# Performance work log

Measured on AMD Instinct MI355X. Metric: run time of the kernel, lower is better.

## Reference

```python
import jax, jax.numpy as jnp
import numpy as np

D_MODEL = 1024
N_INPUT = 4096
N_PROCESS = 2048
D_ROUTING = 256
TEMPERATURE = 0.5
LN_EPS = 1e-5


def _gelu(x):
    return jax.nn.gelu(x, approximate=False)  # torch F.gelu default (erf)


def setup_inputs() -> dict:
    key = jax.random.key(0)
    ks = jax.random.split(key, 10)
    B, S = 8, 2048
    x = jax.random.normal(ks[0], (B, S, D_MODEL), dtype=jnp.float32)
    # GlobalRouter query_net: Linear(d_model, 2*d_routing) -> GELU -> LayerNorm -> Linear(2*d_routing, d_routing)
    W1 = jax.random.normal(ks[1], (2 * D_ROUTING, D_MODEL), dtype=jnp.float32) * (2.0 / (D_MODEL + 2 * D_ROUTING)) ** 0.5 * 1.414
    b1 = jnp.zeros((2 * D_ROUTING,), dtype=jnp.float32)
    ln_g = jnp.ones((2 * D_ROUTING,), dtype=jnp.float32)
    ln_b = jnp.zeros((2 * D_ROUTING,), dtype=jnp.float32)
    W2 = jax.random.normal(ks[2], (D_ROUTING, 2 * D_ROUTING), dtype=jnp.float32) * (2.0 / (3 * D_ROUTING)) ** 0.5 * 1.414
    b2 = jnp.zeros((D_ROUTING,), dtype=jnp.float32)
    neuron_keys = jax.random.normal(ks[3], (N_INPUT, D_ROUTING), dtype=jnp.float32) / D_ROUTING ** 0.5 * 1.414
    input_patterns = jax.random.normal(ks[4], (N_INPUT, D_MODEL), dtype=jnp.float32) / D_MODEL ** 0.5 * 1.414
    process_weights = jax.random.normal(ks[5], (N_PROCESS, N_INPUT), dtype=jnp.float32) / N_INPUT ** 0.5 * 1.414
    process_outputs = jax.random.normal(ks[6], (N_PROCESS, D_MODEL), dtype=jnp.float32) / D_MODEL ** 0.5 * 1.414
    return {
        'x': x, 'k_input': 2048, 'k_process': 1024,
        'W1': W1, 'b1': b1, 'ln_g': ln_g, 'ln_b': ln_b, 'W2': W2, 'b2': b2,
        'neuron_keys': neuron_keys, 'input_patterns': input_patterns,
        'process_weights': process_weights, 'process_outputs': process_outputs,
    }


def _forward(x, k_input, k_process, W1, b1, ln_g, ln_b, W2, b2,
             neuron_keys, input_patterns, process_weights, process_outputs):
    B, S, d_model = x.shape
    # ---- GlobalRouter ----
    gctx = jnp.max(x, axis=1)                                  # [B, d_model]
    h = _gelu(gctx @ W1.T + b1)                                # [B, 2*d_routing]
    mu = jnp.mean(h, axis=-1, keepdims=True)
    var = jnp.mean((h - mu) ** 2, axis=-1, keepdims=True)
    h = (h - mu) * jax.lax.rsqrt(var + LN_EPS) * ln_g + ln_b
    query = h @ W2.T + b2                                      # [B, d_routing]
    logits = (query @ neuron_keys.T) / D_ROUTING ** 0.5        # [B, n_input]
    probs = jax.nn.softmax(logits / TEMPERATURE, axis=-1)
    _, input_idx = jax.lax.top_k(logits, k_input)              # [B, k_input]
    one_hot = jnp.zeros_like(probs).at[jnp.arange(B)[:, None], input_idx].set(1.0)
    routing_weights = jax.lax.stop_gradient(one_hot - probs) + probs  # STE
    # ---- input neuron stage ----
    input_acts = _gelu(jnp.einsum('bsd,nd->bsn', x, input_patterns))   # [B,S,n_input]
    weighted = input_acts * routing_weights[:, None, :]
    sel_in = jnp.take_along_axis(weighted, input_idx[:, None, :], axis=2)  # [B,S,k_input]
    # gather process weight columns per batch: [B, n_process, k_input]
    W_sel = jnp.transpose(process_weights[:, input_idx], (1, 0, 2))
    process_acts = _gelu(jnp.einsum('bsk,bpk->bsp', sel_in, W_sel))    # [B,S,n_process]
    # ---- process neuron stage ----
    process_scores = jnp.mean(process_acts, axis=1)                    # [B,n_process]
    _, process_idx = jax.lax.top_k(process_scores, k_process)          # [B,k_process]
    sel_proc = jnp.take_along_axis(process_acts, process_idx[:, None, :], axis=2)  # [B,S,k_process]
    out_sel = process_outputs[process_idx]                             # [B,k_process,d_model]
    return jnp.einsum('bsp,bpd->bsd', sel_proc, out_sel)


def reference(x, k_input, k_process, W1, b1, ln_g, ln_b, W2, b2,
              neuron_keys, input_patterns, process_weights, process_outputs):
    return _forward(x, k_input, k_process, W1, b1, ln_g, ln_b, W2, b2,
                    neuron_keys, input_patterns, process_weights, process_outputs)
```

## Files before the change

### kernel.cpp

```cpp
#include <hip/hip_runtime.h>
#include <stdint.h>

#define B_  8
#define S_  2048
#define DM  1024
#define NI  4096
#define NP  2048
#define DR  256
#define H2  512
#define KI  2048
#define KP  1024
#define LDW 40

typedef __attribute__((ext_vector_type(8))) short bf16x8;
typedef __attribute__((ext_vector_type(4))) float f32x4;
typedef unsigned short ushort;
typedef unsigned int uint;

__device__ __forceinline__ float gelu_erf(float v){
    return 0.5f * v * (1.0f + erff(v * 0.7071067811865476f));
}
__device__ __forceinline__ ushort f2b(float f){
    union { float f; uint u; } a; a.f = f;
    uint r = a.u + 0x7fffu + ((a.u >> 16) & 1u);
    return (ushort)(r >> 16);
}
__device__ __forceinline__ float b2f(ushort u){
    union { uint u; float f; } a; a.u = ((uint)u) << 16; return a.f;
}
__device__ __forceinline__ void cvt8(const float* p, uint4& H, uint4& L){
    uint h[4], l[4];
    #pragma unroll
    for(int i = 0; i < 4; i++){
        ushort h0 = f2b(p[2*i]);   float f0 = b2f(h0); ushort l0 = f2b(p[2*i]   - f0);
        ushort h1 = f2b(p[2*i+1]); float f1 = b2f(h1); ushort l1 = f2b(p[2*i+1] - f1);
        h[i] = (uint)h0 | ((uint)h1 << 16);
        l[i] = (uint)l0 | ((uint)l1 << 16);
    }
    H = uint4{h[0],h[1],h[2],h[3]};
    L = uint4{l[0],l[1],l[2],l[3]};
}
__device__ __forceinline__ void gload_lds16(const void* g, void* l){
    __builtin_amdgcn_global_load_lds((const __attribute__((address_space(1))) void*)g,
                                     (__attribute__((address_space(3))) void*)l, 16, 0, 0);
}

__global__ __launch_bounds__(256) void k_pre(const float* __restrict__ x,
                                             const float* __restrict__ patt,
                                             const float* __restrict__ pout,
                                             float* __restrict__ gpart,
                                             ushort* __restrict__ xh,
                                             ushort* __restrict__ xl,
                                             ushort* __restrict__ patth,
                                             ushort* __restrict__ pattl,
                                             ushort* __restrict__ poutb){
    int bid = blockIdx.x;
    int t = threadIdx.x;
    if(bid < 256){
        int b = bid >> 5, ch = bid & 31;
        size_t row0 = (size_t)b*S_ + (size_t)ch*64;
        const float4* xb = (const float4*)(x + row0*DM);
        float4 m = float4{-3.402823466e38f, -3.402823466e38f, -3.402823466e38f, -3.402823466e38f};
        for(int r = 0; r < 64; r++){
            float4 v = xb[(size_t)r*(DM/4) + t];
            ushort hx = f2b(v.x), hy = f2b(v.y), hz = f2b(v.z), hw = f2b(v.w);
            uint2 H{ (uint)hx | ((uint)hy << 16), (uint)hz | ((uint)hw << 16) };
            uint2 L{ (uint)f2b(v.x - b2f(hx)) | ((uint)f2b(v.y - b2f(hy)) << 16),
                     (uint)f2b(v.z - b2f(hz)) | ((uint)f2b(v.w - b2f(hw)) << 16) };
            ((uint2*)(xh + (row0 + r)*DM))[t] = H;
            ((uint2*)(xl + (row0 + r)*DM))[t] = L;
            m.x = fmaxf(m.x, v.x); m.y = fmaxf(m.y, v.y);
            m.z = fmaxf(m.z, v.z); m.w = fmaxf(m.w, v.w);
        }
        ((float4*)(gpart + (size_t)(b*32 + ch)*DM))[t] = m;
    }else if(bid < 2304){
        size_t idx = (size_t)(bid - 256)*256 + t;
        float f[8];
        *(float4*)(f)     = ((const float4*)patt)[idx*2];
        *(float4*)(f + 4) = ((const float4*)patt)[idx*2 + 1];
        uint4 H, L; cvt8(f, H, L);
        ((uint4*)patth)[idx] = H;
        ((uint4*)pattl)[idx] = L;
    }else{
        size_t idx = (size_t)(bid - 2304)*256 + t;
        float f[8];
        *(float4*)(f)     = ((const float4*)pout)[idx*2];
        *(float4*)(f + 4) = ((const float4*)pout)[idx*2 + 1];
        uint o[4];
        #pragma unroll
        for(int i = 0; i < 4; i++)
            o[i] = (uint)f2b(f[2*i]) | ((uint)f2b(f[2*i+1]) << 16);
        ((uint4*)poutb)[idx] = uint4{o[0], o[1], o[2], o[3]};
    }
}

__global__ __launch_bounds__(256) void k_h(const float* __restrict__ gpart,
                                           const float* __restrict__ W1,
                                           const float* __restrict__ b1,
                                           float* __restrict__ h){
    __shared__ float g[DM];
    int b = blockIdx.x >> 3, ig = blockIdx.x & 7;
    int t = threadIdx.x;
    for(int d = t; d < DM; d += 256){
        float m = gpart[(size_t)(b*32)*DM + d];
        for(int c = 1; c < 32; c++) m = fmaxf(m, gpart[(size_t)(b*32 + c)*DM + d]);
        g[d] = m;
    }
    __syncthreads();
    int i  = ig*64 + (t >> 2);
    int dq = (t & 3) * 256;
    const float* wr = W1 + (size_t)i*DM + dq;
    const float* gg = g + dq;
    float s = 0.f;
    for(int d = 0; d < 256; d++) s = fmaf(gg[d], wr[d], s);
    s += __shfl_xor(s, 1);
    s += __shfl_xor(s, 2);
    if((t & 3) == 0) h[b*H2 + i] = gelu_erf(s + b1[i]);
}

__global__ __launch_bounds__(256) void k_query(const float* __restrict__ h,
                                               const float* __restrict__ lng,
                                               const float* __restrict__ lnb,
                                               const float* __restrict__ W2,
                                               const float* __restrict__ b2,
                                               float* __restrict__ query){
    __shared__ float hn[H2];
    __shared__ float red[4];
    int b = blockIdx.x >> 2, qg = blockIdx.x & 3;
    int t = threadIdx.x;
    float v0 = h[b*H2 + t], v1 = h[b*H2 + 256 + t];
    float s = v0 + v1;
    for(int o = 32; o > 0; o >>= 1) s += __shfl_down(s, o);
    if((t & 63) == 0) red[t >> 6] = s;
    __syncthreads();
    float mean = (red[0] + red[1] + red[2] + red[3]) * (1.f/H2);
    __syncthreads();
    float d0 = v0 - mean, d1 = v1 - mean;
    float sq = d0*d0 + d1*d1;
    for(int o = 32; o > 0; o >>= 1) sq += __shfl_down(sq, o);
    if((t & 63) == 0) red[t >> 6] = sq;
    __syncthreads();
    float var  = (red[0] + red[1] + red[2] + red[3]) * (1.f/H2);
    float rstd = rsqrtf(var + 1e-5f);
    hn[t]       = d0*rstd*lng[t]       + lnb[t];
    hn[256 + t] = d1*rstd*lng[256 + t] + lnb[256 + t];
    __syncthreads();
    int q  = qg*64 + (t >> 2);
    int iq = (t & 3) * 128;
    const float* wr = W2 + (size_t)q*H2 + iq;
    float acc = 0.f;
    for(int i2 = 0; i2 < 128; i2++) acc = fmaf(hn[iq + i2], wr[i2], acc);
    acc += __shfl_xor(acc, 1);
    acc += __shfl_xor(acc, 2);
    if((t & 3) == 0) query[b*DR + q] = acc + b2[q];
}

__global__ __launch_bounds__(256) void k_logits(const float* __restrict__ query,
                                                const float* __restrict__ nk,
                                                float* __restrict__ logits){
    __shared__ float4 q4[DR/4];
    int b = blockIdx.x >> 5, ng = blockIdx.x & 31;
    int t = threadIdx.x;
    if(t < 64) q4[t] = ((const float4*)(query + (size_t)b*DR))[t];
    __syncthreads();
    int w = t >> 6, lane = t & 63;
    float4 qv = q4[lane];
    int nbase = ng*128 + w*32;
    #pragma unroll 2
    for(int i = 0; i < 32; i++){
        int n = nbase + i;
        float4 v = ((const float4*)(nk + (size_t)n*DR))[lane];
        float p = v.x*qv.x + v.y*qv.y + v.z*qv.z + v.w*qv.w;
        p += __shfl_down(p, 32); p += __shfl_down(p, 16); p += __shfl_down(p, 8);
        p += __shfl_down(p, 4);  p += __shfl_down(p, 2);  p += __shfl_down(p, 1);
        if(lane == 0) logits[(size_t)b*NI + n] = p * 0.0625f;
    }
}

template<int N_, int KSEL>
__global__ __launch_bounds__(1024) void k_topk(const float* __restrict__ vals,
                                               int* __restrict__ idxout){
    __shared__ unsigned u[N_];
    __shared__ int hist[256];
    __shared__ int sfx[512];
    __shared__ int sc[1024];
    __shared__ int sel_d, sel_need;
    int t = threadIdx.x;
    size_t vbase = (size_t)blockIdx.x * N_;
    size_t obase = (size_t)blockIdx.x * KSEL;
    for(int i = t; i < N_; i += 1024){
        unsigned bits = __float_as_uint(vals[vbase + i]);
        u[i] = (bits & 0x80000000u) ? ~bits : (bits | 0x80000000u);
    }
    unsigned long long prefix = 0;
    int need = KSEL;
    for(int bb = 3; bb >= 0; bb--){
        if(t < 256) hist[t] = 0;
        __syncthreads();
        for(int i = t; i < N_; i += 1024){
            unsigned v = u[i];
            if(((unsigned long long)v >> ((bb + 1)*8)) == prefix)
                atomicAdd(&hist[(v >> (bb*8)) & 255], 1);
        }
        __syncthreads();
        if(t < 256) sfx[t] = hist[t];
        else if(t < 512) sfx[t] = 0;
        __syncthreads();
        for(int o = 1; o < 256; o <<= 1){
            int v2 = (t < 256) ? sfx[t + o] : 0;
            __syncthreads();
            if(t < 256) sfx[t] += v2;
            __syncthreads();
        }
        if(t < 256){
            int hi_c = sfx[t + 1];
            if(sfx[t] >= need && hi_c < need){ sel_d = t; sel_need = need - hi_c; }
        }
        __syncthreads();
        prefix = (prefix << 8) | (unsigned)sel_d;
        need = sel_need;
        __syncthreads();
    }
    unsigned T = (unsigned)prefix;
    const int PER = N_ / 1024;
    int base = t * PER;
    int lgt = 0, leq = 0;
    for(int j = 0; j < PER; j++){
        unsigned v = u[base + j];
        lgt += (v > T) ? 1 : 0; leq += (v == T) ? 1 : 0;
    }
    sc[t] = (lgt << 16) | leq;
    __syncthreads();
    for(int o = 1; o < 1024; o <<= 1){
        int add = (t >= o) ? sc[t - o] : 0;
        __syncthreads();
        sc[t] += add;
        __syncthreads();
    }
    int need2 = KSEL - (sc[1023] >> 16);
    int ex = (t == 0) ? 0 : sc[t - 1];
    int pos = (ex >> 16) + ((ex & 0xffff) < need2 ? (ex & 0xffff) : need2);
    int eq = ex & 0xffff;
    for(int j = 0; j < PER; j++){
        unsigned v = u[base + j];
        if(v > T){ idxout[obase + pos++] = base + j; }
        else if(v == T){ if(eq < need2){ idxout[obase + pos++] = base + j; } eq++; }
    }
}

__global__ __launch_bounds__(256) void k_gemm1(const ushort* __restrict__ xh,
                                               const ushort* __restrict__ xl,
                                               const ushort* __restrict__ ph,
                                               const ushort* __restrict__ pl,
                                               const int* __restrict__ iidx,
                                               ushort* __restrict__ selh,
                                               ushort* __restrict__ sell, int b0){
    __shared__ __align__(16) ushort Ah[2][128*32], Al[2][128*32], Bh[2][128*32], Bl[2][128*32];
    __shared__ int rowmap[128];
    int t = threadIdx.x;
    int g = blockIdx.x >> 8, rest = blockIdx.x & 255;
    int b = b0 + g;
    int mb = rest >> 4, nb = rest & 15;
    int m0 = mb*128, n0 = nb*128;
    ushort* selh_g = selh + (size_t)g*S_*KI;
    ushort* sell_g = sell + (size_t)g*S_*KI;
    if(t < 128) rowmap[t] = iidx[(size_t)b*KI + n0 + t];
    __syncthreads();
    int w = t >> 6, l = t & 63;
    int lr = l >> 2, lc = l & 3;
    int r0 = 32*w + lr, r1 = r0 + 16;
    const ushort* pAh0 = xh + ((size_t)b*S_ + m0 + r0)*DM + lc*8;
    const ushort* pAh1 = xh + ((size_t)b*S_ + m0 + r1)*DM + lc*8;
    const ushort* pAl0 = xl + ((size_t)b*S_ + m0 + r0)*DM + lc*8;
    const ushort* pAl1 = xl + ((size_t)b*S_ + m0 + r1)*DM + lc*8;
    const ushort* pBh0 = ph + (size_t)rowmap[r0]*DM + lc*8;
    const ushort* pBh1 = ph + (size_t)rowmap[r1]*DM + lc*8;
    const ushort* pBl0 = pl + (size_t)rowmap[r0]*DM + lc*8;
    const ushort* pBl1 = pl + (size_t)rowmap[r1]*DM + lc*8;
    int d0 = w*1024, d1 = d0 + 512;
    #define STG1(BUF, KO) do{ \
        gload_lds16(pAh0 + (KO), &Ah[BUF][d0]); \
        gload_lds16(pAh1 + (KO), &Ah[BUF][d1]); \
        gload_lds16(pAl0 + (KO), &Al[BUF][d0]); \
        gload_lds16(pAl1 + (KO), &Al[BUF][d1]); \
        gload_lds16(pBh0 + (KO), &Bh[BUF][d0]); \
        gload_lds16(pBh1 + (KO), &Bh[BUF][d1]); \
        gload_lds16(pBl0 + (KO), &Bl[BUF][d0]); \
        gload_lds16(pBl1 + (KO), &Bl[BUF][d1]); \
    }while(0)
    STG1(0, 0);
    int lm = l & 15, q = l >> 4;
    int mbase = (w >> 1)*64, nbase = (w & 1)*64;
    f32x4 acc[4][4];
    #pragma unroll
    for(int i = 0; i < 4; i++)
      #pragma unroll
      for(int j = 0; j < 4; j++) acc[i][j] = f32x4{0.f,0.f,0.f,0.f};
    int cur = 0;
    for(int k0 = 0; k0 < DM; k0 += 32){
        if(k0 + 32 < DM){
            STG1(cur^1, k0 + 32);
            asm volatile("s_waitcnt vmcnt(8)" ::: "memory");
        }else{
            asm volatile("s_waitcnt vmcnt(0)" ::: "memory");
        }
        __builtin_amdgcn_s_barrier();
        asm volatile("" ::: "memory");
        bf16x8 ahf[4], alf[4];
        #pragma unroll
        for(int mt = 0; mt < 4; mt++){
            ahf[mt] = *(const bf16x8*)(&Ah[cur][(mbase + mt*16 + lm)*32 + q*8]);
            alf[mt] = *(const bf16x8*)(&Al[cur][(mbase + mt*16 + lm)*32 + q*8]);
        }
        __builtin_amdgcn_s_setprio(1);
        #pragma unroll
        for(int nt = 0; nt < 4; nt++){
            bf16x8 bhf = *(const bf16x8*)(&Bh[cur][(nbase + nt*16 + lm)*32 + q*8]);
            bf16x8 blf = *(const bf16x8*)(&Bl[cur][(nbase + nt*16 + lm)*32 + q*8]);
            #pragma unroll
            for(int mt = 0; mt < 4; mt++){
                acc[mt][nt] = __builtin_amdgcn_mfma_f32_16x16x32_bf16(ahf[mt], bhf, acc[mt][nt], 0, 0, 0);
                acc[mt][nt] = __builtin_amdgcn_mfma_f32_16x16x32_bf16(ahf[mt], blf, acc[mt][nt], 0, 0, 0);
                acc[mt][nt] = __builtin_amdgcn_mfma_f32_16x16x32_bf16(alf[mt], bhf, acc[mt][nt], 0, 0, 0);
            }
        }
        __builtin_amdgcn_s_setprio(0);
        asm volatile("s_waitcnt lgkmcnt(0)" ::: "memory");
        __builtin_amdgcn_s_barrier();
        asm volatile("" ::: "memory");
        cur ^= 1;
    }
    #undef STG1
    #pragma unroll
    for(int mt = 0; mt < 4; mt++)
      #pragma unroll
      for(int nt = 0; nt < 4; nt++){
        int col = n0 + nbase + nt*16 + lm;
        #pragma unroll
        for(int i = 0; i < 4; i++){
            int row = m0 + mbase + mt*16 + q*4 + i;
            float gv = gelu_erf(acc[mt][nt][i]);
            ushort hbits = f2b(gv);
            selh_g[(size_t)row*KI + col] = hbits;
            sell_g[(size_t)row*KI + col] = f2b(gv - b2f(hbits));
        }
      }
}

__global__ __launch_bounds__(256) void k_gather_wsel(const float* __restrict__ pw,
                                                     const int* __restrict__ iidx,
                                                     ushort* __restrict__ wh,
                                                     ushort* __restrict__ wl,
                                                     float* __restrict__ scores, int b0){
    int g = blockIdx.x >> 8, pc = blockIdx.x & 255;
    int b = b0 + g;
    ushort* wh_g = wh + (size_t)g*NP*KI;
    ushort* wl_g = wl + (size_t)g*NP*KI;
    int t = threadIdx.x;
    if(t < 8) scores[(size_t)b*NP + pc*8 + t] = 0.f;
    int j0 = t*8;
    int k8[8];
    *(int4*)(k8)     = *(const int4*)(iidx + (size_t)b*KI + j0);
    *(int4*)(k8 + 4) = *(const int4*)(iidx + (size_t)b*KI + j0 + 4);
    for(int r2 = 0; r2 < 8; r2++){
        int p = pc*8 + r2;
        const float* row = pw + (size_t)p*NI;
        uint hh[4], ll[4];
        #pragma unroll
        for(int i = 0; i < 4; i++){
            float v0 = row[k8[2*i]], v1 = row[k8[2*i+1]];
            ushort h0 = f2b(v0), h1 = f2b(v1);
            hh[i] = (uint)h0 | ((uint)h1 << 16);
            ll[i] = (uint)f2b(v0 - b2f(h0)) | ((uint)f2b(v1 - b2f(h1)) << 16);
        }
        *(uint4*)(wh_g + (size_t)p*KI + j0) = uint4{hh[0],hh[1],hh[2],hh[3]};
        *(uint4*)(wl_g + (size_t)p*KI + j0) = uint4{ll[0],ll[1],ll[2],ll[3]};
    }
}

__global__ __launch_bounds__(256) void k_gemm2(const ushort* __restrict__ selh,
                                               const ushort* __restrict__ sell,
                                               const ushort* __restrict__ wh,
                                               const ushort* __restrict__ wl,
                                               ushort* __restrict__ acts,
                                               float* __restrict__ scores, int b0){
    __shared__ __align__(16) ushort Ah[2][128*32], Al[2][128*32], Bh[2][128*32], Bl[2][128*32];
    __shared__ float colsum[128];
    int t = threadIdx.x;
    int g = blockIdx.x >> 8, rest = blockIdx.x & 255;
    int b = b0 + g;
    int mb = rest >> 4, nb = rest & 15;
    int m0 = mb*128, n0 = nb*128;
    const ushort* selh_g = selh + (size_t)g*S_*KI;
    const ushort* sell_g = sell + (size_t)g*S_*KI;
    const ushort* wh_g   = wh   + (size_t)g*NP*KI;
    const ushort* wl_g   = wl   + (size_t)g*NP*KI;
    ushort* acts_g = acts + (size_t)g*S_*NP;
    int w = t >> 6, l = t & 63;
    int lr = l >> 2, lc = l & 3;
    int r0 = 32*w + lr, r1 = r0 + 16;
    const ushort* pAh0 = selh_g + (size_t)(m0 + r0)*KI + lc*8;
    const ushort* pAh1 = selh_g + (size_t)(m0 + r1)*KI + lc*8;
    const ushort* pAl0 = sell_g + (size_t)(m0 + r0)*KI + lc*8;
    const ushort* pAl1 = sell_g + (size_t)(m0 + r1)*KI + lc*8;
    const ushort* pBh0 = wh_g + (size_t)(n0 + r0)*KI + lc*8;
    const ushort* pBh1 = wh_g + (size_t)(n0 + r1)*KI + lc*8;
    const ushort* pBl0 = wl_g + (size_t)(n0 + r0)*KI + lc*8;
    const ushort* pBl1 = wl_g + (size_t)(n0 + r1)*KI + lc*8;
    int d0 = w*1024, d1 = d0 + 512;
    #define STG2(BUF, KO) do{ \
        gload_lds16(pAh0 + (KO), &Ah[BUF][d0]); \
        gload_lds16(pAh1 + (KO), &Ah[BUF][d1]); \
        gload_lds16(pAl0 + (KO), &Al[BUF][d0]); \
        gload_lds16(pAl1 + (KO), &Al[BUF][d1]); \
        gload_lds16(pBh0 + (KO), &Bh[BUF][d0]); \
        gload_lds16(pBh1 + (KO), &Bh[BUF][d1]); \
        gload_lds16(pBl0 + (KO), &Bl[BUF][d0]); \
        gload_lds16(pBl1 + (KO), &Bl[BUF][d1]); \
    }while(0)
    STG2(0, 0);
    int lm = l & 15, q = l >> 4;
    int mbase = (w >> 1)*64, nbase = (w & 1)*64;
    f32x4 acc[4][4];
    #pragma unroll
    for(int i = 0; i < 4; i++)
      #pragma unroll
      for(int j = 0; j < 4; j++) acc[i][j] = f32x4{0.f,0.f,0.f,0.f};
    int cur = 0;
    for(int k0 = 0; k0 < KI; k0 += 32){
        if(k0 + 32 < KI){
            STG2(cur^1, k0 + 32);
            asm volatile("s_waitcnt vmcnt(8)" ::: "memory");
        }else{
            asm volatile("s_waitcnt vmcnt(0)" ::: "memory");
        }
        __builtin_amdgcn_s_barrier();
        asm volatile("" ::: "memory");
        bf16x8 ahf[4], alf[4];
        #pragma unroll
        for(int mt = 0; mt < 4; mt++){
            ahf[mt] = *(const bf16x8*)(&Ah[cur][(mbase + mt*16 + lm)*32 + q*8]);
            alf[mt] = *(const bf16x8*)(&Al[cur][(mbase + mt*16 + lm)*32 + q*8]);
        }
        __builtin_amdgcn_s_setprio(1);
        #pragma unroll
        for(int nt = 0; nt < 4; nt++){
            bf16x8 bhf = *(const bf16x8*)(&Bh[cur][(nbase + nt*16 + lm)*32 + q*8]);
            bf16x8 blf = *(const bf16x8*)(&Bl[cur][(nbase + nt*16 + lm)*32 + q*8]);
            #pragma unroll
            for(int mt = 0; mt < 4; mt++){
                acc[mt][nt] = __builtin_amdgcn_mfma_f32_16x16x32_bf16(ahf[mt], bhf, acc[mt][nt], 0, 0, 0);
                acc[mt][nt] = __builtin_amdgcn_mfma_f32_16x16x32_bf16(ahf[mt], blf, acc[mt][nt], 0, 0, 0);
                acc[mt][nt] = __builtin_amdgcn_mfma_f32_16x16x32_bf16(alf[mt], bhf, acc[mt][nt], 0, 0, 0);
            }
        }
        __builtin_amdgcn_s_setprio(0);
        asm volatile("s_waitcnt lgkmcnt(0)" ::: "memory");
        __builtin_amdgcn_s_barrier();
        asm volatile("" ::: "memory");
        cur ^= 1;
    }
    #undef STG2
    if(t < 128) colsum[t] = 0.f;
    __syncthreads();
    #pragma unroll
    for(int mt = 0; mt < 4; mt++)
      #pragma unroll
      for(int nt = 0; nt < 4; nt++){
        int cb = nbase + nt*16 + lm;
        float s4 = 0.f;
        #pragma unroll
        for(int i = 0; i < 4; i++){
            int row = m0 + mbase + mt*16 + q*4 + i;
            float gv = gelu_erf(acc[mt][nt][i]);
            s4 += gv;
            acts_g[(size_t)row*NP + n0 + cb] = f2b(gv);
        }
        atomicAdd(&colsum[cb], s4);
      }
    __syncthreads();
    if(t < 128) atomicAdd(&scores[(size_t)b*NP + n0 + t], colsum[t]);
}

__global__ __launch_bounds__(256) void k_gather_selacts(const ushort* __restrict__ acts,
                                                        const int* __restrict__ pidx,
                                                        ushort* __restrict__ selacts, int b0){
    int g = blockIdx.x >> 6, sc_ = blockIdx.x & 63;
    int b = b0 + g;
    const ushort* acts_g = acts + (size_t)g*S_*NP;
    ushort* selacts_g = selacts + (size_t)g*S_*KP;
    int t = threadIdx.x;
    int j0 = t*4;
    int4 p4 = *(const int4*)(pidx + (size_t)b*KP + j0);
    const ushort* Ab = acts_g    + ((size_t)sc_*32)*NP;
    ushort*       Ob = selacts_g + ((size_t)sc_*32)*KP;
    for(int r2 = 0; r2 < 32; r2++){
        const ushort* Ar = Ab + (size_t)r2*NP;
        ushort o0 = Ar[p4.x], o1 = Ar[p4.y], o2 = Ar[p4.z], o3 = Ar[p4.w];
        uint2 ov{ (uint)o0 | ((uint)o1 << 16), (uint)o2 | ((uint)o3 << 16) };
        *(uint2*)(Ob + (size_t)r2*KP + j0) = ov;
    }
}

__global__ __launch_bounds__(256) void k_gemm3(const ushort* __restrict__ selacts,
                                               const ushort* __restrict__ poutb,
                                               const int* __restrict__ pidx,
                                               float* __restrict__ out, int b0){
    __shared__ __align__(16) ushort As[2][128*32];
    __shared__ __align__(16) ushort Bs[2][128*LDW];
    __shared__ int pix[KP];
    int t = threadIdx.x;
    int g = blockIdx.x >> 7, rest = blockIdx.x & 127;
    int b = b0 + g;
    int mb = rest >> 3, nb = rest & 7;
    int m0 = mb*128, n0 = nb*128;
    const ushort* sel_g = selacts + (size_t)g*S_*KP;
    int w = t >> 6, l = t & 63;
    int lr = l >> 2, lc = l & 3;
    int r0 = 32*w + lr, r1 = r0 + 16;
    const ushort* pA0 = sel_g + (size_t)(m0 + r0)*KP + lc*8;
    const ushort* pA1 = sel_g + (size_t)(m0 + r1)*KP + lc*8;
    int d0 = w*1024, d1 = d0 + 512;
    gload_lds16(pA0, &As[0][d0]);
    gload_lds16(pA1, &As[0][d1]);
    for(int i = t; i < KP; i += 256) pix[i] = pidx[(size_t)b*KP + i];
    __syncthreads();
    int kk = t >> 3, nc = (t & 7)*16;
    uint4 B0, B1;
    {
        const ushort* bg = poutb + (size_t)pix[kk]*DM + n0 + nc;
        B0 = *(const uint4*)(bg); B1 = *(const uint4*)(bg + 8);
    }
    int lm = l & 15, q = l >> 4;
    int mbase = (w >> 1)*64, nbase = (w & 1)*64;
    f32x4 acc[4][4];
    #pragma unroll
    for(int i = 0; i < 4; i++)
      #pragma unroll
      for(int j = 0; j < 4; j++) acc[i][j] = f32x4{0.f,0.f,0.f,0.f};
    for(int k0 = 0; k0 < KP; k0 += 32){
        int cur = (k0 >> 5) & 1;
        {
            const ushort* pb0 = (const ushort*)&B0;
            const ushort* pb1 = (const ushort*)&B1;
            #pragma unroll
            for(int c = 0; c < 8; c++) Bs[cur][(nc + c)*LDW + kk]     = pb0[c];
            #pragma unroll
            for(int c = 0; c < 8; c++) Bs[cur][(nc + 8 + c)*LDW + kk] = pb1[c];
        }
        if(k0 + 32 < KP){
            gload_lds16(pA0 + (k0 + 32), &As[cur^1][d0]);
            gload_lds16(pA1 + (k0 + 32), &As[cur^1][d1]);
            asm volatile("s_waitcnt vmcnt(2)" ::: "memory");
        }else{
            asm volatile("s_waitcnt vmcnt(0)" ::: "memory");
        }
        asm volatile("s_waitcnt lgkmcnt(0)" ::: "memory");
        __builtin_amdgcn_s_barrier();
        asm volatile("" ::: "memory");
        if(k0 + 32 < KP){
            const ushort* bg = poutb + (size_t)pix[k0 + 32 + kk]*DM + n0 + nc;
            B0 = *(const uint4*)(bg); B1 = *(const uint4*)(bg + 8);
        }
        bf16x8 af[4];
        #pragma unroll
        for(int mt = 0; mt < 4; mt++)
            af[mt] = *(const bf16x8*)(&As[cur][(mbase + mt*16 + lm)*32 + q*8]);
        __builtin_amdgcn_s_setprio(1);
        #pragma unroll
        for(int nt = 0; nt < 4; nt++){
            bf16x8 bf = *(const bf16x8*)(&Bs[cur][(nbase + nt*16 + lm)*LDW + q*8]);
            #pragma unroll
            for(int mt = 0; mt < 4; mt++)
                acc[mt][nt] = __builtin_amdgcn_mfma_f32_16x16x32_bf16(af[mt], bf, acc[mt][nt], 0, 0, 0);
        }
        __builtin_amdgcn_s_setprio(0);
        asm volatile("s_waitcnt lgkmcnt(0)" ::: "memory");
        __builtin_amdgcn_s_barrier();
        asm volatile("" ::: "memory");
    }
    float* Cb = out + (size_t)b*S_*DM;
    #pragma unroll
    for(int mt = 0; mt < 4; mt++)
      #pragma unroll
      for(int nt = 0; nt < 4; nt++){
        int col = n0 + nbase + nt*16 + lm;
        #pragma unroll
        for(int i = 0; i < 4; i++){
            int row = m0 + mbase + mt*16 + q*4 + i;
            Cb[(size_t)row*DM + col] = acc[mt][nt][i];
        }
      }
}

extern "C" void kernel_launch(void* const* d_in, const int* in_sizes, int n_in,
                              void* d_out, int out_size, void* d_ws, size_t ws_size,
                              hipStream_t stream){
    const float* x    = (const float*)d_in[0];
    const float* W1   = (const float*)d_in[3];
    const float* b1   = (const float*)d_in[4];
    const float* lng  = (const float*)d_in[5];
    const float* lnb  = (const float*)d_in[6];
    const float* W2   = (const float*)d_in[7];
    const float* b2   = (const float*)d_in[8];
    const float* nk   = (const float*)d_in[9];
    const float* patt = (const float*)d_in[10];
    const float* pw   = (const float*)d_in[11];
    const float* pout = (const float*)d_in[12];
    float* out = (float*)d_out;

    auto al256 = [](size_t v){ return (v + 255) & ~(size_t)255; };
    const size_t fixed =
        al256((size_t)B_*32*DM*4) + al256((size_t)B_*H2*4) + al256((size_t)B_*DR*4) +
        al256((size_t)B_*NI*4)    + al256((size_t)B_*KI*4) + al256((size_t)B_*NP*4) +
        al256((size_t)B_*KP*4) +
        2*al256((size_t)B_*S_*DM*2) + 2*al256((size_t)NI*DM*2) + al256((size_t)NP*DM*2);
    const size_t perb = (size_t)S_*KI*2*2 + (size_t)NP*KI*2*2 + (size_t)S_*NP*2 + (size_t)S_*KP*2 + 6*256;
    int G = 8;
    while(G > 1 && fixed + (size_t)G*perb > ws_size) G >>= 1;
    if(fixed + (size_t)G*perb > ws_size) return;

    char* wsp = (char*)d_ws;
    size_t off = 0;
    auto alloc = [&](size_t bytes) -> void* {
        void* p = wsp + off;
        off += (bytes + 255) & ~(size_t)255;
        return p;
    };
    float*  gpart   = (float*) alloc((size_t)B_*32*DM*4);
    float*  h       = (float*) alloc((size_t)B_*H2*4);
    float*  query   = (float*) alloc((size_t)B_*DR*4);
    float*  logits  = (float*) alloc((size_t)B_*NI*4);
    int*    iidx    = (int*)   alloc((size_t)B_*KI*4);
    float*  scores  = (float*) alloc((size_t)B_*NP*4);
    int*    pidx    = (int*)   alloc((size_t)B_*KP*4);
    ushort* xh      = (ushort*)alloc((size_t)B_*S_*DM*2);
    ushort* xl      = (ushort*)alloc((size_t)B_*S_*DM*2);
    ushort* patth   = (ushort*)alloc((size_t)NI*DM*2);
    ushort* pattl   = (ushort*)alloc((size_t)NI*DM*2);
    ushort* poutb   = (ushort*)alloc((size_t)NP*DM*2);
    ushort* selh    = (ushort*)alloc((size_t)G*S_*KI*2);
    ushort* sell    = (ushort*)alloc((size_t)G*S_*KI*2);
    ushort* wselh   = (ushort*)alloc((size_t)G*NP*KI*2);
    ushort* wsell   = (ushort*)alloc((size_t)G*NP*KI*2);
    ushort* acts    = (ushort*)alloc((size_t)G*S_*NP*2);
    ushort* selacts = (ushort*)alloc((size_t)G*S_*KP*2);

    dim3 blk(256);
    k_pre   <<<3328, blk, 0, stream>>>(x, patt, pout, gpart, xh, xl, patth, pattl, poutb);
    k_h     <<<64,  blk, 0, stream>>>(gpart, W1, b1, h);
    k_query <<<32,  blk, 0, stream>>>(h, lng, lnb, W2, b2, query);
    k_logits<<<B_*32, blk, 0, stream>>>(query, nk, logits);
    k_topk<NI, KI><<<B_, dim3(1024), 0, stream>>>(logits, iidx);
    for(int b0 = 0; b0 < B_; b0 += G){
        k_gemm1        <<<G*256, blk, 0, stream>>>(xh, xl, patth, pattl, iidx, selh, sell, b0);
        k_gather_wsel  <<<G*256, blk, 0, stream>>>(pw, iidx, wselh, wsell, scores, b0);
        k_gemm2        <<<G*256, blk, 0, stream>>>(selh, sell, wselh, wsell, acts, scores, b0);
        k_topk<NP, KP> <<<G,     dim3(1024), 0, stream>>>(scores + (size_t)b0*NP, pidx + (size_t)b0*KP);
        k_gather_selacts<<<G*64, blk, 0, stream>>>(acts, pidx, selacts, b0);
        k_gemm3        <<<G*128, blk, 0, stream>>>(selacts, poutb, pidx, out, b0);
    }
}
```

Baseline: 1.334 ms.

## Widen gemm1/gemm2 tiles to 128x256 with XOR-swizzled LDS layout

The first two split-bf16 GEMMs now use 128x256 block tiles, with each wave owning a 128x64 strip instead of a 64x64 quadrant. This halves the grid and raises operand reuse per LDS load. LDS rows are XOR-swizzled on both the global-to-LDS staging and the fragment reads, to reduce bank conflicts. In exchange, the block uses roughly double the LDS and 128 accumulator registers per lane with launch_bounds(256,1), which lowers occupancy, and there are fewer blocks to spread across CUs.

```diff
diff --git a/kernel.cpp b/kernel.cpp
--- a/kernel.cpp
+++ b/kernel.cpp
@@ -248,80 +248,90 @@
     }
 }
 
-__global__ __launch_bounds__(256) void k_gemm1(const ushort* __restrict__ xh,
-                                               const ushort* __restrict__ xl,
-                                               const ushort* __restrict__ ph,
-                                               const ushort* __restrict__ pl,
-                                               const int* __restrict__ iidx,
-                                               ushort* __restrict__ selh,
-                                               ushort* __restrict__ sell, int b0){
-    __shared__ __align__(16) ushort Ah[2][128*32], Al[2][128*32], Bh[2][128*32], Bl[2][128*32];
-    __shared__ int rowmap[128];
-    int t = threadIdx.x;
-    int g = blockIdx.x >> 8, rest = blockIdx.x & 255;
+__global__ __launch_bounds__(256, 1) void k_gemm1(const ushort* __restrict__ xh,
+                                                  const ushort* __restrict__ xl,
+                                                  const ushort* __restrict__ ph,
+                                                  const ushort* __restrict__ pl,
+                                                  const int* __restrict__ iidx,
+                                                  ushort* __restrict__ selh,
+                                                  ushort* __restrict__ sell, int b0){
+    __shared__ __align__(16) ushort Ah[2][4096], Al[2][4096], Bh[2][8192], Bl[2][8192];
+    __shared__ int rowmap[256];
+    int t = threadIdx.x;
+    int g = blockIdx.x >> 7, rest = blockIdx.x & 127;
     int b = b0 + g;
-    int mb = rest >> 4, nb = rest & 15;
-    int m0 = mb*128, n0 = nb*128;
+    int mb = rest >> 3, nb = rest & 7;
+    int m0 = mb*128, n0 = nb*256;
     ushort* selh_g = selh + (size_t)g*S_*KI;
     ushort* sell_g = sell + (size_t)g*S_*KI;
-    if(t < 128) rowmap[t] = iidx[(size_t)b*KI + n0 + t];
+    rowmap[t] = iidx[(size_t)b*KI + n0 + t];
     __syncthreads();
     int w = t >> 6, l = t & 63;
     int lr = l >> 2, lc = l & 3;
-    int r0 = 32*w + lr, r1 = r0 + 16;
-    const ushort* pAh0 = xh + ((size_t)b*S_ + m0 + r0)*DM + lc*8;
-    const ushort* pAh1 = xh + ((size_t)b*S_ + m0 + r1)*DM + lc*8;
-    const ushort* pAl0 = xl + ((size_t)b*S_ + m0 + r0)*DM + lc*8;
-    const ushort* pAl1 = xl + ((size_t)b*S_ + m0 + r1)*DM + lc*8;
-    const ushort* pBh0 = ph + (size_t)rowmap[r0]*DM + lc*8;
-    const ushort* pBh1 = ph + (size_t)rowmap[r1]*DM + lc*8;
-    const ushort* pBl0 = pl + (size_t)rowmap[r0]*DM + lc*8;
-    const ushort* pBl1 = pl + (size_t)rowmap[r1]*DM + lc*8;
-    int d0 = w*1024, d1 = d0 + 512;
+    int ra = w*16 + lr;
+    int cs = lc ^ ((ra >> 1) & 3);
+    const ushort* pAh0 = xh + ((size_t)b*S_ + m0 + ra)*DM + cs*8;
+    const ushort* pAh1 = xh + ((size_t)b*S_ + m0 + ra + 64)*DM + cs*8;
+    const ushort* pAl0 = xl + ((size_t)b*S_ + m0 + ra)*DM + cs*8;
+    const ushort* pAl1 = xl + ((size_t)b*S_ + m0 + ra + 64)*DM + cs*8;
+    int rB0 = rowmap[ra], rB1 = rowmap[ra + 64], rB2 = rowmap[ra + 128], rB3 = rowmap[ra + 192];
+    const ushort* pBh0 = ph + (size_t)rB0*DM + cs*8;
+    const ushort* pBh1 = ph + (size_t)rB1*DM + cs*8;
+    const ushort* pBh2 = ph + (size_t)rB2*DM + cs*8;
+    const ushort* pBh3 = ph + (size_t)rB3*DM + cs*8;
+    const ushort* pBl0 = pl + (size_t)rB0*DM + cs*8;
+    const ushort* pBl1 = pl + (size_t)rB1*DM + cs*8;
+    const ushort* pBl2 = pl + (size_t)rB2*DM + cs*8;
+    const ushort* pBl3 = pl + (size_t)rB3*DM + cs*8;
+    int dA = w*512;
     #define STG1(BUF, KO) do{ \
-        gload_lds16(pAh0 + (KO), &Ah[BUF][d0]); \
-        gload_lds16(pAh1 + (KO), &Ah[BUF][d1]); \
-        gload_lds16(pAl0 + (KO), &Al[BUF][d0]); \
-        gload_lds16(pAl1 + (KO), &Al[BUF][d1]); \
-        gload_lds16(pBh0 + (KO), &Bh[BUF][d0]); \
-        gload_lds16(pBh1 + (KO), &Bh[BUF][d1]); \
-        gload_lds16(pBl0 + (KO), &Bl[BUF][d0]); \
-        gload_lds16(pBl1 + (KO), &Bl[BUF][d1]); \
+        gload_lds16(pAh0 + (KO), &Ah[BUF][dA]); \
+        gload_lds16(pAh1 + (KO), &Ah[BUF][2048 + dA]); \
+        gload_lds16(pAl0 + (KO), &Al[BUF][dA]); \
+        gload_lds16(pAl1 + (KO), &Al[BUF][2048 + dA]); \
+        gload_lds16(pBh0 + (KO), &Bh[BUF][dA]); \
+        gload_lds16(pBh1 + (KO), &Bh[BUF][2048 + dA]); \
+        gload_lds16(pBh2 + (KO), &Bh[BUF][4096 + dA]); \
+        gload_lds16(pBh3 + (KO), &Bh[BUF][6144 + dA]); \
+        gload_lds16(pBl0 + (KO), &Bl[BUF][dA]); \
+        gload_lds16(pBl1 + (KO), &Bl[BUF][2048 + dA]); \
+        gload_lds16(pBl2 + (KO), &Bl[BUF][4096 + dA]); \
+        gload_lds16(pBl3 + (KO), &Bl[BUF][6144 + dA]); \
     }while(0)
     STG1(0, 0);
     int lm = l & 15, q = l >> 4;
-    int mbase = (w >> 1)*64, nbase = (w & 1)*64;
-    f32x4 acc[4][4];
+    int xq = (q ^ ((lm >> 1) & 3)) * 8;
+    f32x4 acc[8][4];
     #pragma unroll
-    for(int i = 0; i < 4; i++)
+    for(int i = 0; i < 8; i++)
       #pragma unroll
       for(int j = 0; j < 4; j++) acc[i][j] = f32x4{0.f,0.f,0.f,0.f};
     int cur = 0;
     for(int k0 = 0; k0 < DM; k0 += 32){
         if(k0 + 32 < DM){
             STG1(cur^1, k0 + 32);
-            asm volatile("s_waitcnt vmcnt(8)" ::: "memory");
+            asm volatile("s_waitcnt vmcnt(12)" ::: "memory");
         }else{
             asm volatile("s_waitcnt vmcnt(0)" ::: "memory");
         }
         __builtin_amdgcn_s_barrier();
         asm volatile("" ::: "memory");
-        bf16x8 ahf[4], alf[4];
-        #pragma unroll
-        for(int mt = 0; mt < 4; mt++){
-            ahf[mt] = *(const bf16x8*)(&Ah[cur][(mbase + mt*16 + lm)*32 + q*8]);
-            alf[mt] = *(const bf16x8*)(&Al[cur][(mbase + mt*16 + lm)*32 + q*8]);
+        bf16x8 bhf[4], blf[4];
+        #pragma unroll
+        for(int nt = 0; nt < 4; nt++){
+            bhf[nt] = *(const bf16x8*)(&Bh[cur][(w*64 + nt*16 + lm)*32 + xq]);
+            blf[nt] = *(const bf16x8*)(&Bl[cur][(w*64 + nt*16 + lm)*32 + xq]);
         }
         __builtin_amdgcn_s_setprio(1);
         #pragma unroll
-        for(int nt = 0; nt < 4; nt++){
-            bf16x8 bhf = *(const bf16x8*)(&Bh[cur][(nbase + nt*16 + lm)*32 + q*8]);
-            bf16x8 blf = *(const bf16x8*)(&Bl[cur][(nbase + nt*16 + lm)*32 + q*8]);
+        for(int mt = 0; mt < 8; mt++){
+            bf16x8 ahf = *(const bf16x8*)(&Ah[cur][(mt*16 + lm)*32 + xq]);
+            bf16x8 alf = *(const bf16x8*)(&Al[cur][(mt*16 + lm)*32 + xq]);
             #pragma unroll
-            for(int mt = 0; mt < 4; mt++){
-                acc[mt][nt] = __builtin_amdgcn_mfma_f32_16x16x32_bf16(ahf[mt], bhf, acc[mt][nt], 0, 0, 0);
-                acc[mt][nt] = __builtin_amdgcn_mfma_f32_16x16x32_bf16(ahf[mt], blf, acc[mt][nt], 0, 0, 0);
-                acc[mt][nt] = __builtin_amdgcn_mfma_f32_16x16x32_bf16(alf[mt], bhf, acc[mt][nt], 0, 0, 0);
+            for(int nt = 0; nt < 4; nt++){
+                acc[mt][nt] = __builtin_amdgcn_mfma_f32_16x16x32_bf16(ahf, bhf[nt], acc[mt][nt], 0, 0, 0);
+                acc[mt][nt] = __builtin_amdgcn_mfma_f32_16x16x32_bf16(ahf, blf[nt], acc[mt][nt], 0, 0, 0);
+                acc[mt][nt] = __builtin_amdgcn_mfma_f32_16x16x32_bf16(alf, bhf[nt], acc[mt][nt], 0, 0, 0);
             }
         }
         __builtin_amdgcn_s_setprio(0);
@@ -332,13 +342,13 @@
     }
     #undef STG1
     #pragma unroll
-    for(int mt = 0; mt < 4; mt++)
+    for(int mt = 0; mt < 8; mt++)
       #pragma unroll
       for(int nt = 0; nt < 4; nt++){
-        int col = n0 + nbase + nt*16 + lm;
+        int col = n0 + w*64 + nt*16 + lm;
         #pragma unroll
         for(int i = 0; i < 4; i++){
-            int row = m0 + mbase + mt*16 + q*4 + i;
+            int row = m0 + mt*16 + q*4 + i;
             float gv = gelu_erf(acc[mt][nt][i]);
             ushort hbits = f2b(gv);
             selh_g[(size_t)row*KI + col] = hbits;
@@ -378,19 +388,19 @@
     }
 }
 
-__global__ __launch_bounds__(256) void k_gemm2(const ushort* __restrict__ selh,
-                                               const ushort* __restrict__ sell,
-                                               const ushort* __restrict__ wh,
-                                               const ushort* __restrict__ wl,
-                                               ushort* __restrict__ acts,
-                                               float* __restrict__ scores, int b0){
-    __shared__ __align__(16) ushort Ah[2][128*32], Al[2][128*32], Bh[2][128*32], Bl[2][128*32];
-    __shared__ float colsum[128];
-    int t = threadIdx.x;
-    int g = blockIdx.x >> 8, rest = blockIdx.x & 255;
+__global__ __launch_bounds__(256, 1) void k_gemm2(const ushort* __restrict__ selh,
+                                                  const ushort* __restrict__ sell,
+                                                  const ushort* __restrict__ wh,
+                                                  const ushort* __restrict__ wl,
+                                                  ushort* __restrict__ acts,
+                                                  float* __restrict__ scores, int b0){
+    __shared__ __align__(16) ushort Ah[2][4096], Al[2][4096], Bh[2][8192], Bl[2][8192];
+    __shared__ float colsum[256];
+    int t = threadIdx.x;
+    int g = blockIdx.x >> 7, rest = blockIdx.x & 127;
     int b = b0 + g;
-    int mb = rest >> 4, nb = rest & 15;
-    int m0 = mb*128, n0 = nb*128;
+    int mb = rest >> 3, nb = rest & 7;
+    int m0 = mb*128, n0 = nb*256;
     const ushort* selh_g = selh + (size_t)g*S_*KI;
     const ushort* sell_g = sell + (size_t)g*S_*KI;
     const ushort* wh_g   = wh   + (size_t)g*NP*KI;
@@ -398,60 +408,69 @@
     ushort* acts_g = acts + (size_t)g*S_*NP;
     int w = t >> 6, l = t & 63;
     int lr = l >> 2, lc = l & 3;
-    int r0 = 32*w + lr, r1 = r0 + 16;
-    const ushort* pAh0 = selh_g + (size_t)(m0 + r0)*KI + lc*8;
-    const ushort* pAh1 = selh_g + (size_t)(m0 + r1)*KI + lc*8;
-    const ushort* pAl0 = sell_g + (size_t)(m0 + r0)*KI + lc*8;
-    const ushort* pAl1 = sell_g + (size_t)(m0 + r1)*KI + lc*8;
-    const ushort* pBh0 = wh_g + (size_t)(n0 + r0)*KI + lc*8;
-    const ushort* pBh1 = wh_g + (size_t)(n0 + r1)*KI + lc*8;
-    const ushort* pBl0 = wl_g + (size_t)(n0 + r0)*KI + lc*8;
-    const ushort* pBl1 = wl_g + (size_t)(n0 + r1)*KI + lc*8;
-    int d0 = w*1024, d1 = d0 + 512;
+    int ra = w*16 + lr;
+    int cs = lc ^ ((ra >> 1) & 3);
+    const ushort* pAh0 = selh_g + (size_t)(m0 + ra)*KI + cs*8;
+    const ushort* pAh1 = selh_g + (size_t)(m0 + ra + 64)*KI + cs*8;
+    const ushort* pAl0 = sell_g + (size_t)(m0 + ra)*KI + cs*8;
+    const ushort* pAl1 = sell_g + (size_t)(m0 + ra + 64)*KI + cs*8;
+    const ushort* pBh0 = wh_g + (size_t)(n0 + ra)*KI + cs*8;
+    const ushort* pBh1 = wh_g + (size_t)(n0 + ra + 64)*KI + cs*8;
+    const ushort* pBh2 = wh_g + (size_t)(n0 + ra + 128)*KI + cs*8;
+    const ushort* pBh3 = wh_g + (size_t)(n0 + ra + 192)*KI + cs*8;
+    const ushort* pBl0 = wl_g + (size_t)(n0 + ra)*KI + cs*8;
+    const ushort* pBl1 = wl_g + (size_t)(n0 + ra + 64)*KI + cs*8;
+    const ushort* pBl2 = wl_g + (size_t)(n0 + ra + 128)*KI + cs*8;
+    const ushort* pBl3 = wl_g + (size_t)(n0 + ra + 192)*KI + cs*8;
+    int dA = w*512;
     #define STG2(BUF, KO) do{ \
-        gload_lds16(pAh0 + (KO), &Ah[BUF][d0]); \
-        gload_lds16(pAh1 + (KO), &Ah[BUF][d1]); \
-        gload_lds16(pAl0 + (KO), &Al[BUF][d0]); \
-        gload_lds16(pAl1 + (KO), &Al[BUF][d1]); \
-        gload_lds16(pBh0 + (KO), &Bh[BUF][d0]); \
-        gload_lds16(pBh1 + (KO), &Bh[BUF][d1]); \
-        gload_lds16(pBl0 + (KO), &Bl[BUF][d0]); \
-        gload_lds16(pBl1 + (KO), &Bl[BUF][d1]); \
+        gload_lds16(pAh0 + (KO), &Ah[BUF][dA]); \
+        gload_lds16(pAh1 + (KO), &Ah[BUF][2048 + dA]); \
+        gload_lds16(pAl0 + (KO), &Al[BUF][dA]); \
+        gload_lds16(pAl1 + (KO), &Al[BUF][2048 + dA]); \
+        gload_lds16(pBh0 + (KO), &Bh[BUF][dA]); \
+        gload_lds16(pBh1 + (KO), &Bh[BUF][2048 + dA]); \
+        gload_lds16(pBh2 + (KO), &Bh[BUF][4096 + dA]); \
+        gload_lds16(pBh3 + (KO), &Bh[BUF][6144 + dA]); \
+        gload_lds16(pBl0 + (KO), &Bl[BUF][dA]); \
+        gload_lds16(pBl1 + (KO), &Bl[BUF][2048 + dA]); \
+        gload_lds16(pBl2 + (KO), &Bl[BUF][4096 + dA]); \
+        gload_lds16(pBl3 + (KO), &Bl[BUF][6144 + dA]); \
     }while(0)
     STG2(0, 0);
     int lm = l & 15, q = l >> 4;
-    int mbase = (w >> 1)*64, nbase = (w & 1)*64;
-    f32x4 acc[4][4];
+    int xq = (q ^ ((lm >> 1) & 3)) * 8;
+    f32x4 acc[8][4];
     #pragma unroll
-    for(int i = 0; i < 4; i++)
+    for(int i = 0; i < 8; i++)
       #pragma unroll
       for(int j = 0; j < 4; j++) acc[i][j] = f32x4{0.f,0.f,0.f,0.f};
     int cur = 0;
     for(int k0 = 0; k0 < KI; k0 += 32){
         if(k0 + 32 < KI){
             STG2(cur^1, k0 + 32);
-            asm volatile("s_waitcnt vmcnt(8)" ::: "memory");
+            asm volatile("s_waitcnt vmcnt(12)" ::: "memory");
         }else{
             asm volatile("s_waitcnt vmcnt(0)" ::: "memory");
         }
         __builtin_amdgcn_s_barrier();
         asm volatile("" ::: "memory");
-        bf16x8 ahf[4], alf[4];
-        #pragma unroll
-        for(int mt = 0; mt < 4; mt++){
-            ahf[mt] = *(const bf16x8*)(&Ah[cur][(mbase + mt*16 + lm)*32 + q*8]);
-            alf[mt] = *(const bf16x8*)(&Al[cur][(mbase + mt*16 + lm)*32 + q*8]);
+        bf16x8 bhf[4], blf[4];
+        #pragma unroll
+        for(int nt = 0; nt < 4; nt++){
+            bhf[nt] = *(const bf16x8*)(&Bh[cur][(w*64 + nt*16 + lm)*32 + xq]);
+            blf[nt] = *(const bf16x8*)(&Bl[cur][(w*64 + nt*16 + lm)*32 + xq]);
         }
         __builtin_amdgcn_s_setprio(1);
         #pragma unroll
-        for(int nt = 0; nt < 4; nt++){
-            bf16x8 bhf = *(const bf16x8*)(&Bh[cur][(nbase + nt*16 + lm)*32 + q*8]);
-            bf16x8 blf = *(const bf16x8*)(&Bl[cur][(nbase + nt*16 + lm)*32 + q*8]);
+        for(int mt = 0; mt < 8; mt++){
+            bf16x8 ahf = *(const bf16x8*)(&Ah[cur][(mt*16 + lm)*32 + xq]);
+            bf16x8 alf = *(const bf16x8*)(&Al[cur][(mt*16 + lm)*32 + xq]);
             #pragma unroll
-            for(int mt = 0; mt < 4; mt++){
-                acc[mt][nt] = __builtin_amdgcn_mfma_f32_16x16x32_bf16(ahf[mt], bhf, acc[mt][nt], 0, 0, 0);
-                acc[mt][nt] = __builtin_amdgcn_mfma_f32_16x16x32_bf16(ahf[mt], blf, acc[mt][nt], 0, 0, 0);
-                acc[mt][nt] = __builtin_amdgcn_mfma_f32_16x16x32_bf16(alf[mt], bhf, acc[mt][nt], 0, 0, 0);
+            for(int nt = 0; nt < 4; nt++){
+                acc[mt][nt] = __builtin_amdgcn_mfma_f32_16x16x32_bf16(ahf, bhf[nt], acc[mt][nt], 0, 0, 0);
+                acc[mt][nt] = __builtin_amdgcn_mfma_f32_16x16x32_bf16(ahf, blf[nt], acc[mt][nt], 0, 0, 0);
+                acc[mt][nt] = __builtin_amdgcn_mfma_f32_16x16x32_bf16(alf, bhf[nt], acc[mt][nt], 0, 0, 0);
             }
         }
         __builtin_amdgcn_s_setprio(0);
@@ -461,17 +480,17 @@
         cur ^= 1;
     }
     #undef STG2
-    if(t < 128) colsum[t] = 0.f;
+    colsum[t] = 0.f;
     __syncthreads();
     #pragma unroll
-    for(int mt = 0; mt < 4; mt++)
+    for(int mt = 0; mt < 8; mt++)
       #pragma unroll
       for(int nt = 0; nt < 4; nt++){
-        int cb = nbase + nt*16 + lm;
+        int cb = w*64 + nt*16 + lm;
         float s4 = 0.f;
         #pragma unroll
         for(int i = 0; i < 4; i++){
-            int row = m0 + mbase + mt*16 + q*4 + i;
+            int row = m0 + mt*16 + q*4 + i;
             float gv = gelu_erf(acc[mt][nt][i]);
             s4 += gv;
             acts_g[(size_t)row*NP + n0 + cb] = f2b(gv);
@@ -479,7 +498,7 @@
         atomicAdd(&colsum[cb], s4);
       }
     __syncthreads();
-    if(t < 128) atomicAdd(&scores[(size_t)b*NP + n0 + t], colsum[t]);
+    atomicAdd(&scores[(size_t)b*NP + n0 + t], colsum[t]);
 }
 
 __global__ __launch_bounds__(256) void k_gather_selacts(const ushort* __restrict__ acts,
@@ -653,9 +672,9 @@
     k_logits<<<B_*32, blk, 0, stream>>>(query, nk, logits);
     k_topk<NI, KI><<<B_, dim3(1024), 0, stream>>>(logits, iidx);
     for(int b0 = 0; b0 < B_; b0 += G){
-        k_gemm1        <<<G*256, blk, 0, stream>>>(xh, xl, patth, pattl, iidx, selh, sell, b0);
+        k_gemm1        <<<G*128, blk, 0, stream>>>(xh, xl, patth, pattl, iidx, selh, sell, b0);
         k_gather_wsel  <<<G*256, blk, 0, stream>>>(pw, iidx, wselh, wsell, scores, b0);
-        k_gemm2        <<<G*256, blk, 0, stream>>>(selh, sell, wselh, wsell, acts, scores, b0);
+        k_gemm2        <<<G*128, blk, 0, stream>>>(selh, sell, wselh, wsell, acts, scores, b0);
         k_topk<NP, KP> <<<G,     dim3(1024), 0, stream>>>(scores + (size_t)b0*NP, pidx + (size_t)b0*KP);
         k_gather_selacts<<<G*64, blk, 0, stream>>>(acts, pidx, selacts, b0);
         k_gemm3        <<<G*128, blk, 0, stream>>>(selacts, poutb, pidx, out, b0);
```

Result: slower. 1.548 ms (+16.1%).
